# Performance work log

Hardware: AMD Instinct MI355X
Metric: run time of the kernel (lower is better)

Reference implementation:

```python
import jax, jax.numpy as jnp
import numpy as np

T, N, HID = 128, 128, 64
H_, W_ = 8, 8
CONV_OUT = H_ * W_ * HID  # 4096
N_SUB = 5
A, B, C = 5, 3, 6          # subtask_space = task_space.nvec[0]
SUB_SIZE = A + B + C       # 14
N_G = A * B * C            # 90
STATE = N_SUB + SUB_SIZE + HID + SUB_SIZE + 1 + 1  # 99
D_IN = CONV_OUT + 3 * N_SUB  # 4111


def setup_inputs() -> dict:
    key = jax.random.key(0)
    ks = jax.random.split(key, 16)
    sc = 0.02
    obs = jax.random.normal(ks[0], (T, N, CONV_OUT), jnp.float32)
    task_type = jax.random.randint(ks[1], (T, N, N_SUB), 0, A).astype(jnp.float32)
    count = jax.random.randint(ks[2], (T, N, N_SUB), 1, B + 1).astype(jnp.float32)
    obj = jax.random.randint(ks[3], (T, N, N_SUB), 0, C).astype(jnp.float32)
    inp = jnp.concatenate([obs, task_type, count, obj], axis=-1)  # [T,N,4111]
    hx = jnp.zeros((1, N, STATE), jnp.float32)
    return {
        "input": inp,
        "hx": hx,
        "Wf": jax.random.normal(ks[4], (HID, CONV_OUT + 2 * SUB_SIZE + 1), jnp.float32) * sc,
        "bf": jnp.zeros((HID,), jnp.float32),
        "Wih": jax.random.normal(ks[5], (3 * HID, 2 * HID), jnp.float32) * sc,
        "bih": jnp.zeros((3 * HID,), jnp.float32),
        "bhh": jnp.zeros((3 * HID,), jnp.float32),
        "Wc": jax.random.normal(ks[6], (1, 2 * HID), jnp.float32) * sc,
        "bc": jnp.zeros((1,), jnp.float32),
        "Wl": jax.random.normal(ks[7], (3, HID), jnp.float32) * sc,
        "bl": jnp.zeros((3,), jnp.float32),
        "Wpi": jax.random.normal(ks[8], (N_G, HID + SUB_SIZE), jnp.float32) * sc,
        "bpi": jnp.zeros((N_G,), jnp.float32),
        "Wb": jax.random.normal(ks[9], (2, CONV_OUT + SUB_SIZE), jnp.float32) * sc,
        "bb": jnp.zeros((2,), jnp.float32),
    }


def _forward(input, hx, Wf, bf, Wih, bih, bhh, Wc, bc, Wl, bl, Wpi, bpi, Wb, bb):
    obs = input[..., :CONV_OUT]
    tt = input[..., CONV_OUT:CONV_OUT + N_SUB].astype(jnp.int32)
    cnt = input[..., CONV_OUT + N_SUB:CONV_OUT + 2 * N_SUB].astype(jnp.int32) - 1
    obj = input[..., CONV_OUT + 2 * N_SUB:].astype(jnp.int32)

    ea, eb, ec = jnp.eye(A, dtype=input.dtype), jnp.eye(B, dtype=input.dtype), jnp.eye(C, dtype=input.dtype)

    def embed(t1, t2, t3):
        return jnp.concatenate([ea[t1], eb[t2], ec[t3]], axis=-1)

    M = embed(tt[0], cnt[0], obj[0])  # [N, N_SUB, SUB_SIZE]

    # parse hidden state
    h0_all = hx[0]
    i0, i1, i2, i3, i4 = np.cumsum([N_SUB, SUB_SIZE, HID, SUB_SIZE, 1])
    p0, r0, h0, g0, b0 = (h0_all[:, :i0], h0_all[:, i0:i1], h0_all[:, i1:i2],
                          h0_all[:, i2:i3], h0_all[:, i3:i4])

    new_ep = jnp.all(hx == 0)
    p0 = jnp.where(new_ep, p0.at[:, 0].set(1.0), p0)
    r0 = jnp.where(new_ep, M[:, 0], r0)
    g0 = jnp.where(new_ep, M[:, 0], g0)

    bhr, bhz, bhn = jnp.split(bhh, 3)
    keys = jax.random.split(jax.random.key(42), input.shape[0])

    def step(carry, xs):
        p_, r_, h_, g_, bprev = carry
        x, k = xs
        s = jnp.concatenate([x, r_, g_, bprev], axis=-1) @ Wf.T + bf   # f (linear)
        sh = jnp.concatenate([s, h_], axis=-1)
        cg = jax.nn.sigmoid(sh @ Wc.T + bc)                             # [N,1] phi_update
        # GRUCell called with hidden=None -> zero hidden state
        gi = sh @ Wih.T + bih
        gr, gz, gn = jnp.split(gi, 3, axis=-1)
        rg = jax.nn.sigmoid(gr + bhr)
        z = jax.nn.sigmoid(gz + bhz)
        n = jnp.tanh(gn + rg * bhn)
        hnew = (1.0 - z) * n
        # shift attention: per-batch conv1d(p, l, padding=1)
        l = jax.nn.softmax(h_ @ Wl.T + bl, axis=-1)                     # [N,3]
        pp = jnp.pad(p_, ((0, 0), (1, 1)))
        pconv = pp[:, :-2] * l[:, :1] + pp[:, 1:-1] * l[:, 1:2] + pp[:, 2:] * l[:, 2:]
        rnew = jnp.einsum('nk,nks->ns', pconv, M)
        p = cg * pconv + (1.0 - cg) * p_
        r = cg * rnew + (1.0 - cg) * r_
        h = cg * hnew + (1.0 - cg) * h_
        # pi_theta categorical over prod(subtask_space)
        lg = jnp.concatenate([h, r], axis=-1) @ Wpi.T + bpi
        k1, k2 = jax.random.split(k)
        g_idx = jax.random.categorical(k1, lg)                          # [N]
        lp_g = jnp.take_along_axis(jax.nn.log_softmax(lg, axis=-1), g_idx[:, None], axis=1)
        t1 = g_idx // (B * C)
        rem = g_idx % (B * C)
        gemb = embed(t1, rem // C, rem % C)                             # [N, SUB_SIZE]
        g = cg * gemb + (1.0 - cg) * g_
        # beta categorical over 2
        lbeta = jnp.concatenate([x, g], axis=-1) @ Wb.T + bb
        b_idx = jax.random.categorical(k2, lbeta)
        lp_b = jnp.take_along_axis(jax.nn.log_softmax(lbeta, axis=-1), b_idx[:, None], axis=1)
        bflt = b_idx[:, None].astype(p.dtype)
        out = jnp.concatenate([p, r, h, g, bflt, lp_g + lp_b], axis=-1)  # [N, STATE]
        return (p, r, h, g, bflt), out

    _, outs = jax.lax.scan(step, (p0, r0, h0, g0, b0), (obs, keys))
    return outs  # [T, N, STATE]


def reference(input, hx, Wf, bf, Wih, bih, bhh, Wc, bc, Wl, bl, Wpi, bpi, Wb, bb):
    outs = _forward(input, hx, Wf, bf, Wih, bih, bhh, Wc, bc, Wl, bl, Wpi, bpi, Wb, bb)
    return outs, outs[-1]
```

## Files before the change

### kernel.cpp

```cpp
#include <hip/hip_runtime.h>
#include <stdint.h>
#include <math.h>

#define T_STEPS 128
#define NB      128
#define HID     64
#define CONVOUT 4096
#define NSUB    5
#define SUBSZ   14
#define NG      90
#define STATE   99
#define DIN     4111
#define WFCOLS  4125
#define WBCOLS  4110
#define NROWS   (T_STEPS * NB)

__device__ __forceinline__ void tf2x32(unsigned k0, unsigned k1,
                                       unsigned x0, unsigned x1,
                                       unsigned &o0, unsigned &o1) {
  unsigned K0 = k0, K1 = k1, K2 = k0 ^ k1 ^ 0x1BD11BDAu;
  x0 += K0; x1 += K1;
  const int R0[4] = {13, 15, 26, 6};
  const int R1[4] = {17, 29, 16, 24};
  #pragma unroll
  for (int j = 0; j < 4; ++j) { x0 += x1; x1 = (x1 << R0[j]) | (x1 >> (32 - R0[j])); x1 ^= x0; }
  x0 += K1; x1 += K2 + 1u;
  #pragma unroll
  for (int j = 0; j < 4; ++j) { x0 += x1; x1 = (x1 << R1[j]) | (x1 >> (32 - R1[j])); x1 ^= x0; }
  x0 += K2; x1 += K0 + 2u;
  #pragma unroll
  for (int j = 0; j < 4; ++j) { x0 += x1; x1 = (x1 << R0[j]) | (x1 >> (32 - R0[j])); x1 ^= x0; }
  x0 += K0; x1 += K1 + 3u;
  #pragma unroll
  for (int j = 0; j < 4; ++j) { x0 += x1; x1 = (x1 << R1[j]) | (x1 >> (32 - R1[j])); x1 ^= x0; }
  x0 += K1; x1 += K2 + 4u;
  #pragma unroll
  for (int j = 0; j < 4; ++j) { x0 += x1; x1 = (x1 << R0[j]) | (x1 >> (32 - R0[j])); x1 ^= x0; }
  x0 += K2; x1 += K0 + 5u;
  o0 = x0; o1 = x1;
}

__device__ __forceinline__ double bits_to_gumbel_d(unsigned bits) {
  float f = __uint_as_float((bits >> 9) | 0x3f800000u) - 1.0f;
  const double tiny = (double)1.17549435e-38f;
  double u = fmax(tiny, (double)f + tiny);
  return -log(-log(u));
}

__device__ __forceinline__ float rlane(float v, int l) {
  return __int_as_float(__builtin_amdgcn_readlane(__float_as_int(v), l));
}

__device__ __forceinline__ void bar_lds() {
  __asm__ volatile("" ::: "memory");
  __builtin_amdgcn_s_waitcnt(0xC07F);
  __builtin_amdgcn_s_barrier();
  __asm__ volatile("" ::: "memory");
}

__global__ void k_transpose(const float* __restrict__ Wf, const float* __restrict__ Wb,
                            float* __restrict__ Wt) {
  int idx = blockIdx.x * 256 + threadIdx.x;
  int c = idx >> 12;
  int k = idx & 4095;
  float v = (c < 64) ? Wf[(size_t)c * WFCOLS + k] : Wb[(size_t)(c - 64) * WBCOLS + k];
  Wt[(size_t)k * 68 + c] = v;
}

__global__ __launch_bounds__(256, 4) void k_gemm(const float* __restrict__ inp,
                                                 const float* __restrict__ Wt,
                                                 float* __restrict__ Pf,
                                                 double* __restrict__ Pd) {
  __shared__ __align__(16) float xs[64 * 132];
  __shared__ double redd[2][64][2];
  int tid = threadIdx.x;
  int r = tid & 63;
  int w = __builtin_amdgcn_readfirstlane(tid >> 6);
  int rg = blockIdx.x >> 2, kq = blockIdx.x & 3;
  int rowbase = rg * 64;

  float acc[64];
  #pragma unroll
  for (int c = 0; c < 64; ++c) acc[c] = 0.f;
  double ad0 = 0.0, ad1 = 0.0;

  int s_rr[8], s_c4[8];
  #pragma unroll
  for (int i = 0; i < 8; ++i) {
    int idx = tid + i * 256;
    s_rr[i] = idx >> 5;
    s_c4[i] = idx & 31;
  }

  for (int kt = 0; kt < 8; ++kt) {
    int kb = kq * 1024 + kt * 128;
    #pragma unroll
    for (int i = 0; i < 8; ++i) {
      const float* g = inp + (size_t)(rowbase + s_rr[i]) * DIN + kb + s_c4[i] * 4;
      float4 v;
// ... 38 lines not shown
    float* d = red + (size_t)r * 65;
    #pragma unroll
    for (int c = 0; c < 64; ++c) d[c] = acc[c];
    redd[0][r][0] = ad0; redd[0][r][1] = ad1;
  }
  __syncthreads();
  if (w == 0) {
    const float* s = red + (size_t)r * 65;
    #pragma unroll
    for (int c = 0; c < 64; ++c) acc[c] += s[c];
    ad0 += redd[0][r][0]; ad1 += redd[0][r][1];
    int row = rowbase + r;
    float* po = Pf + (size_t)kq * NROWS * 64 + (size_t)row * 64;
    #pragma unroll
    for (int c = 0; c < 64; ++c) po[c] = acc[c];
    Pd[(size_t)kq * NROWS * 2 + (size_t)row * 2 + 0] = ad0;
    Pd[(size_t)kq * NROWS * 2 + (size_t)row * 2 + 1] = ad1;
  }
}

__global__ void k_reduce(const float* __restrict__ Pf, const double* __restrict__ Pd,
                         float* __restrict__ Xf, double* __restrict__ Xb) {
  size_t gid = (size_t)blockIdx.x * 256 + threadIdx.x;
  const size_t NF = (size_t)NROWS * 64;
  if (gid < NF) {
    Xf[gid] = (Pf[gid] + Pf[NF + gid]) + (Pf[2 * NF + gid] + Pf[3 * NF + gid]);
  } else if (gid < NF + (size_t)NROWS * 2) {
    size_t j = gid - NF;
    const size_t ND = (size_t)NROWS * 2;
    Xb[j] = (Pd[j] + Pd[ND + j]) + (Pd[2 * ND + j] + Pd[3 * ND + j]);
  }
}

__global__ void k_noise(double* __restrict__ Gg, double* __restrict__ Gb) {
  int t = blockIdx.x, tid = threadIdx.x;
  unsigned a, b, k1a, k1b, k2a, k2b, o0, o1;
  tf2x32(0u, 42u, 0u, (unsigned)t, a, b);
  tf2x32(a, b, 0u, 0u, k1a, k1b);
  tf2x32(a, b, 0u, 1u, k2a, k2b);
  for (int i = tid; i < NB * NG; i += 256) {
    tf2x32(k1a, k1b, 0u, (unsigned)i, o0, o1);
    Gg[(size_t)t * NB * NG + i] = bits_to_gumbel_d(o0 ^ o1);
  }
  {
    int i = tid;
    tf2x32(k2a, k2b, 0u, (unsigned)i, o0, o1);
    Gb[(size_t)t * NB * 2 + i] = bits_to_gumbel_d(o0 ^ o1);
  }
}

__global__ __launch_bounds__(256) void k_scan(
    const float* __restrict__ inp, const float* __restrict__ hx,
    const float* __restrict__ Wf, const float* __restrict__ bf,
    const float* __restrict__ Wih, const float* __restrict__ bih,
    const float* __restrict__ bhh, const float* __restrict__ Wc,
    const float* __restrict__ bc, const float* __restrict__ Wl,
    const float* __restrict__ bl, const float* __restrict__ Wpi,
    const float* __restrict__ bpi, const float* __restrict__ Wb,
    const float* __restrict__ bb,
    const float* __restrict__ Xf, const double* __restrict__ Xb,
    const double* __restrict__ Gg, const double* __restrict__ Gb,
    float* __restrict__ lgst, float* __restrict__ lbst,
    int* __restrict__ gidxst, int* __restrict__ bidxst,
    float* __restrict__ out) {
  const int n = blockIdx.x;
  const int tid = threadIdx.x;
  const int lane = tid & 63;
  const int w = __builtin_amdgcn_readfirstlane(tid >> 6);

  __shared__ float s_lds[64], h_lds[64], gi_lds[192];
  __shared__ int nz_sh;

  float wih_r[128];
  float bih_r = 0.f;
  if (w != 0) {
    int m = tid - 64;
    #pragma unroll
    for (int k = 0; k < 128; ++k) wih_r[k] = Wih[(size_t)m * 128 + k];
    bih_r = bih[m];
  }

  float wfs[29], wpi0[78], wpi1[78], mtr[5];
  float bf_r = 0, bhr_r = 0, bhz_r = 0, bhn_r = 0;
  float wc0 = 0, wc1 = 0, wl0 = 0, wl1 = 0, wl2 = 0;
  float bl0 = 0, bl1 = 0, bl2 = 0, bc0 = 0, bpi0 = 0, bpi1 = 0;
  float wbs0 = 0, wbs1 = 0;
  float hreg = 0.f, rgbp = 0.f, xf = 0.f;
  double S0 = 0.0, S1 = 0.0, bb0d = 0.0, bb1d = 0.0;
  double gum0 = 0.0, gum1 = 0.0, xb0 = 0.0, xb1 = 0.0, gb0 = 0.0, gb1 = 0.0;
  int dsto = -1;

  if (tid == 0) nz_sh = 0;
  __syncthreads();
  {
    int any = 0;
    const float4* h4 = (const float4*)hx;
    for (int i = tid; i < (NB * STATE) / 4; i += 256) {
      float4 v = h4[i];
      any |= (v.x != 0.f) | (v.y != 0.f) | (v.z != 0.f) | (v.w != 0.f);
    }
    if (any) nz_sh = 1;
  }
  if (w == 0) {
    #pragma unroll
    for (int k = 0; k < 29; ++k) wfs[k] = Wf[(size_t)lane * WFCOLS + CONVOUT + k];
    #pragma unroll
    for (int k = 0; k < 78; ++k) wpi0[k] = Wpi[(size_t)lane * 78 + k];
    bpi0 = bpi[lane];
    if (lane < 26) {
      #pragma unroll
      for (int k = 0; k < 78; ++k) wpi1[k] = Wpi[(size_t)(64 + lane) * 78 + k];
      bpi1 = bpi[64 + lane];
    }
    bf_r = bf[lane];
    bhr_r = bhh[lane]; bhz_r = bhh[64 + lane]; bhn_r = bhh[128 + lane];
    wc0 = Wc[lane]; wc1 = Wc[64 + lane]; bc0 = bc[0];
    wl0 = Wl[lane]; wl1 = Wl[64 + lane]; wl2 = Wl[128 + lane];
    bl0 = bl[0]; bl1 = bl[1]; bl2 = bl[2];
    bb0d = (double)bb[0]; bb1d = (double)bb[1];
    if (lane < 14) { wbs0 = Wb[CONVOUT + lane]; wbs1 = Wb[(size_t)WBCOLS + CONVOUT + lane]; }
    const float* r0 = inp + (size_t)n * DIN + CONVOUT;
    #pragma unroll
    for (int k = 0; k < 5; ++k) {
      int ttv = (int)r0[k], cntv = (int)r0[5 + k] - 1, objv = (int)r0[10 + k];
      float v = 0.f;
      if (lane < 5)       v = (lane == ttv) ? 1.f : 0.f;
      else if (lane < 8)  v = ((lane - 5) == cntv) ? 1.f : 0.f;
      else if (lane < 14) v = ((lane - 8) == objv) ? 1.f : 0.f;
      mtr[k] = v;
    }
    int src = -1;
    if (lane < 14)       { dsto = 5 + lane;          src = dsto; }
    else if (lane < 28)  { dsto = 83 + (lane - 14);  src = dsto; }
    else if (lane == 28) { dsto = 97;                src = 97; }
    else if (lane < 34)  { dsto = lane - 29;         src = dsto; }
    rgbp = (src >= 0) ? hx[(size_t)n * STATE + src] : 0.f;
    hreg = hx[(size_t)n * STATE + 19 + lane];
  }
  __syncthreads();
  if (w == 0) {
    if (nz_sh == 0) {
      const float* r0 = inp + (size_t)n * DIN + CONVOUT;
      int tt0 = (int)r0[0], cnt0 = (int)r0[5] - 1, obj0 = (int)r0[10];
      if (lane == 29) rgbp = 1.f;
      else if (lane < 14) rgbp = mtr[0];
      else if (lane >= 14 && lane < 28) {
        int j = lane - 14;
        rgbp = (j < 5) ? ((j == tt0) ? 1.f : 0.f)
             : (j < 8) ? (((j - 5) == cnt0) ? 1.f : 0.f)
                       : (((j - 8) == obj0) ? 1.f : 0.f);
      }
    }
    #pragma unroll
    for (int j = 0; j < 14; ++j) {
      double gv = (double)rlane(rgbp, 14 + j);
      S0 += gv * (double)rlane(wbs0, j);
      S1 += gv * (double)rlane(wbs1, j);
    }
    h_lds[lane] = hreg;
    gum0 = Gg[(size_t)n * NG + lane];
    gum1 = (lane < 26) ? Gg[(size_t)n * NG + 64 + lane] : 0.0;
    xf = Xf[(size_t)n * 64 + lane];
    xb0 = Xb[(size_t)n * 2 + 0]; xb1 = Xb[(size_t)n * 2 + 1];
    gb0 = Gb[(size_t)n * 2 + 0]; gb1 = Gb[(size_t)n * 2 + 1];
  }
  __syncthreads();

  const size_t outF = (size_t)T_STEPS * NB * STATE;

  #pragma unroll 1
  for (int t = 0; t < T_STEPS; ++t) {
    float sv_own = 0.f, cg = 0.f, accR0 = 0.f, accR1 = 0.f;
    double cgd = 0.0;

    if (w == 0) {
      float acc = xf + bf_r;
      #pragma unroll
      for (int k = 0; k < 29; ++k) acc = fmaf(wfs[k], rlane(rgbp, k), acc);
      sv_own = acc;
      s_lds[lane] = acc;
    }
    bar_lds();

    if (w == 0) {
      float p0 = wl0 * hreg, p1 = wl1 * hreg, p2 = wl2 * hreg;
      float cga = fmaf(wc1, hreg, wc0 * sv_own);
      #pragma unroll
      for (int off = 32; off; off >>= 1) {
        p0 += __shfl_xor(p0, off, 64);
        p1 += __shfl_xor(p1, off, 64);
        p2 += __shfl_xor(p2, off, 64);
        cga += __shfl_xor(cga, off, 64);
      }
      p0 += bl0; p1 += bl1; p2 += bl2;
      float mx = fmaxf(p0, fmaxf(p1, p2));
      float e0 = expf(p0 - mx), e1 = expf(p1 - mx), e2 = expf(p2 - mx);
      float se = e0 + e1 + e2;
      float l0 = e0 / se, l1 = e1 / se, l2 = e2 / se;
      cg = 1.f / (1.f + expf(-(cga + bc0)));
      cgd = (double)cg;
      float pv0 = rlane(rgbp, 29), pv1 = rlane(rgbp, 30), pv2 = rlane(rgbp, 31);
      float pv3 = rlane(rgbp, 32), pv4 = rlane(rgbp, 33);
      float pc0 = pv0 * l1 + pv1 * l2;
      float pc1 = pv0 * l0 + pv1 * l1 + pv2 * l2;
      float pc2 = pv1 * l0 + pv2 * l1 + pv3 * l2;
      float pc3 = pv2 * l0 + pv3 * l1 + pv4 * l2;
      float pc4 = pv3 * l0 + pv4 * l1;
      if (lane >= 29 && lane < 34) {
        float pcl = (lane == 29) ? pc0 : (lane == 30) ? pc1 : (lane == 31) ? pc2
                  : (lane == 32) ? pc3 : pc4;
        rgbp = cg * pcl + (1.f - cg) * rgbp;
      }
      if (lane < 14) {
        float rn = pc0 * mtr[0] + pc1 * mtr[1] + pc2 * mtr[2] + pc3 * mtr[3] + pc4 * mtr[4];
        rgbp = cg * rn + (1.f - cg) * rgbp;
      }
      #pragma unroll
      for (int k = 0; k < 14; ++k) {
        float rv = rlane(rgbp, k);
        accR0 = fmaf(wpi0[64 + k], rv, accR0);
        accR1 = fmaf(wpi1[64 + k], rv, accR1);
      }
    } else {
      float sv = s_lds[lane];
      float hv = h_lds[lane];
      float acc = bih_r;
      #pragma unroll
      for (int k = 0; k < 64; ++k) acc = fmaf(wih_r[k], rlane(sv, k), acc);
      #pragma unroll
      for (int k = 0; k < 64; ++k) acc = fmaf(wih_r[64 + k], rlane(hv, k), acc);
      gi_lds[tid - 64] = acc;
    }
    bar_lds();

    if (w == 0) {
      int tn = (t + 1 < T_STEPS) ? t + 1 : t;
      double gum0n = Gg[(size_t)tn * NB * NG + (size_t)n * NG + lane];
      double gum1n = (lane < 26) ? Gg[(size_t)tn * NB * NG + (size_t)n * NG + 64 + lane] : 0.0;
      float xfn = Xf[((size_t)tn * NB + n) * 64 + lane];
      double xb0n = Xb[((size_t)tn * NB + n) * 2 + 0];
      double xb1n = Xb[((size_t)tn * NB + n) * 2 + 1];
      double gb0n = Gb[((size_t)tn * NB + n) * 2 + 0];
      double gb1n = Gb[((size_t)tn * NB + n) * 2 + 1];

      float g0 = gi_lds[lane], g1 = gi_lds[64 + lane], g2 = gi_lds[128 + lane];
      float rg = 1.f / (1.f + expf(-(g0 + bhr_r)));
      float z  = 1.f / (1.f + expf(-(g1 + bhz_r)));
      float nn = tanhf(g2 + rg * bhn_r);
      float hnew = (1.f - z) * nn;
      hreg = cg * hnew + (1.f - cg) * hreg;

      float a0 = bpi0 + accR0, a1 = bpi1 + accR1;
      #pragma unroll
      for (int k = 0; k < 64; ++k) {
        float hv2 = rlane(hreg, k);
        a0 = fmaf(wpi0[k], hv2, a0);
        a1 = fmaf(wpi1[k], hv2, a1);
      }
      const float NEGINF = -3.0e38f;
      float vb0 = (float)(gum0 + (double)a0);
      float vb1 = (lane < 26) ? (float)(gum1 + (double)a1) : NEGINF;
      float m1, m2; int idx;
      if (vb1 > vb0) { m1 = vb1; idx = lane + 64; m2 = vb0; }
      else           { m1 = vb0; idx = lane;      m2 = vb1; }
      #pragma unroll
      for (int off = 32; off; off >>= 1) {
        float o1 = __shfl_xor(m1, off, 64);
        int   oi = __shfl_xor(idx, off, 64);
        float o2 = __shfl_xor(m2, off, 64);
        bool take = (o1 > m1) || (o1 == m1 && oi < idx);
        float base2 = take ? m1 : m2;
        float oth   = take ? o2 : o1;
        m2 = fmaxf(base2, oth);
        if (take) { m1 = o1; idx = oi; }
      }
      int gidx = idx;
      if (m1 - m2 < 3e-5f) {
        double e0d = (double)bpi0;
        double e1d = (lane < 26) ? (double)bpi1 : -1.0e300;
        #pragma unroll 1
        for (int k = 0; k < 64; ++k) {
          double hv2 = (double)rlane(hreg, k);
          e0d = fma((double)Wpi[(size_t)lane * 78 + k], hv2, e0d);
          if (lane < 26) e1d = fma((double)Wpi[(size_t)(64 + lane) * 78 + k], hv2, e1d);
        }
        #pragma unroll 1
        for (int k = 0; k < 14; ++k) {
          double rv = (double)rlane(rgbp, k);
          e0d = fma((double)Wpi[(size_t)lane * 78 + 64 + k], rv, e0d);
          if (lane < 26) e1d = fma((double)Wpi[(size_t)(64 + lane) * 78 + 64 + k], rv, e1d);
        }
        double kk0 = e0d + gum0;
        double kk1 = (lane < 26) ? e1d + gum1 : -1.0e300;
        double d1; int di;
        if (kk1 > kk0) { d1 = kk1; di = lane + 64; } else { d1 = kk0; di = lane; }
        #pragma unroll
        for (int off = 32; off; off >>= 1) {
          double od = __shfl_xor(d1, off, 64);
          int    oi = __shfl_xor(di, off, 64);
          if (od > d1 || (od == d1 && oi < di)) { d1 = od; di = oi; }
        }
        gidx = di;
      }
      int t1 = gidx / 18, rem = gidx - t1 * 18;
      int b1 = rem / 6, c1 = rem - b1 * 6;
      if (lane >= 14 && lane < 28) {
        int j = lane - 14;
        float ge = (j < 5) ? ((j == t1) ? 1.f : 0.f)
                 : (j < 8) ? (((j - 5) == b1) ? 1.f : 0.f)
                           : (((j - 8) == c1) ? 1.f : 0.f);
        rgbp = cg * ge + (1.f - cg) * rgbp;
      }
      double u0 = (double)rlane(wbs0, t1) + (double)rlane(wbs0, 5 + b1) + (double)rlane(wbs0, 8 + c1);
      double u1 = (double)rlane(wbs1, t1) + (double)rlane(wbs1, 5 + b1) + (double)rlane(wbs1, 8 + c1);
      S0 = cgd * u0 + (1.0 - cgd) * S0;
      S1 = cgd * u1 + (1.0 - cgd) * S1;
      double lb0 = xb0 + bb0d + S0;
      double lb1 = xb1 + bb1d + S1;
      int bi = ((lb1 + gb1) > (lb0 + gb0)) ? 1 : 0;
      if (lane == 28) rgbp = (float)bi;

      size_t rn = (size_t)t * NB + n;
      float* ob = out + rn * STATE;
      if (dsto >= 0) ob[dsto] = rgbp;
      ob[19 + lane] = hreg;
      lgst[rn * NG + lane] = a0;
      if (lane < 26) lgst[rn * NG + 64 + lane] = a1;
      if (lane == 0) {
        lbst[rn * 2 + 0] = (float)lb0; lbst[rn * 2 + 1] = (float)lb1;
        gidxst[rn] = gidx; bidxst[rn] = bi;
      }
      if (t == T_STEPS - 1) {
        float* of = out + outF + (size_t)n * STATE;
        if (dsto >= 0) of[dsto] = rgbp;
        of[19 + lane] = hreg;
      }
      h_lds[lane] = hreg;
      gum0 = gum0n; gum1 = gum1n; xf = xfn;
      xb0 = xb0n; xb1 = xb1n; gb0 = gb0n; gb1 = gb1n;
    }
  }
}

__global__ __launch_bounds__(256) void k_lp(const float* __restrict__ lgst,
                                            const float* __restrict__ lbst,
                                            const int* __restrict__ gidxst,
                                            const int* __restrict__ bidxst,
                                            float* __restrict__ out) {
  int tid = threadIdx.x, lane = tid & 63, w = tid >> 6;
  size_t rn = (size_t)blockIdx.x * 4 + w;
  const float* lg = lgst + rn * NG;
  float v0 = lg[lane];
  float v1 = (lane < 26) ? lg[64 + lane] : -3.0e38f;
  float ml = fmaxf(v0, v1);
  #pragma unroll
  for (int off = 32; off; off >>= 1) ml = fmaxf(ml, __shfl_xor(ml, off, 64));
  float e = expf(v0 - ml) + ((lane < 26) ? expf(v1 - ml) : 0.f);
  #pragma unroll
  for (int off = 32; off; off >>= 1) e += __shfl_xor(e, off, 64);
  int gi = gidxst[rn];
  float lpg = (lg[gi] - ml) - logf(e);
  float lb0 = lbst[rn * 2 + 0], lb1 = lbst[rn * 2 + 1];
  int bi = bidxst[rn];
  float mx = fmaxf(lb0, lb1);
  float seb = expf(lb0 - mx) + expf(lb1 - mx);
  float lpb = ((bi ? lb1 : lb0) - mx) - logf(seb);
  if (lane == 0) {
    int t = (int)(rn / NB), n = (int)(rn % NB);
    float lp = lpg + lpb;
    out[rn * STATE + 98] = lp;
    if (t == T_STEPS - 1) out[(size_t)T_STEPS * NB * STATE + (size_t)n * STATE + 98] = lp;
  }
}

extern "C" void kernel_launch(void* const* d_in, const int* in_sizes, int n_in,
                              void* d_out, int out_size, void* d_ws, size_t ws_size,
                              hipStream_t stream) {
  const float* inp = (const float*)d_in[0];
  const float* hx  = (const float*)d_in[1];
  const float* Wf  = (const float*)d_in[2];
  const float* bf  = (const float*)d_in[3];
  const float* Wih = (const float*)d_in[4];
  const float* bih = (const float*)d_in[5];
  const float* bhh = (const float*)d_in[6];
  const float* Wc  = (const float*)d_in[7];
  const float* bc  = (const float*)d_in[8];
  const float* Wl  = (const float*)d_in[9];
  const float* bl  = (const float*)d_in[10];
  const float* Wpi = (const float*)d_in[11];
  const float* bpi = (const float*)d_in[12];
  const float* Wb  = (const float*)d_in[13];
  const float* bb  = (const float*)d_in[14];
  float* out = (float*)d_out;

  double* Gg = (double*)d_ws;
  double* Gb = Gg + (size_t)T_STEPS * NB * NG;
  double* Xb = Gb + (size_t)T_STEPS * NB * 2;
  double* Pd = Xb + (size_t)NROWS * 2;
  float*  Wt = (float*)(Pd + (size_t)4 * NROWS * 2);
  float*  Xf = Wt + (size_t)4096 * 68;
  float*  Pf = Xf + (size_t)NROWS * 64;
  float*  lgst = Pf;
  float*  lbst = lgst + (size_t)NROWS * NG;
  int*    gidxst = (int*)(lbst + (size_t)NROWS * 2);
  int*    bidxst = gidxst + NROWS;

  k_transpose<<<(66 * 4096) / 256, 256, 0, stream>>>(Wf, Wb, Wt);
  k_gemm<<<1024, 256, 0, stream>>>(inp, Wt, Pf, Pd);
  {
    size_t tot = (size_t)NROWS * 64 + (size_t)NROWS * 2;
    k_reduce<<<(int)((tot + 255) / 256), 256, 0, stream>>>(Pf, Pd, Xf, Xb);
  }
  k_noise<<<T_STEPS, 256, 0, stream>>>(Gg, Gb);
  k_scan<<<NB, 256, 0, stream>>>(inp, hx, Wf, bf, Wih, bih, bhh, Wc, bc, Wl, bl,
                                 Wpi, bpi, Wb, bb, Xf, Xb, Gg, Gb,
                                 lgst, lbst, gidxst, bidxst, out);
  k_lp<<<NROWS / 4, 256, 0, stream>>>(lgst, lbst, gidxst, bidxst, out);
}
```

Measured before the change: 963.0 us.

## Precompute input-side GRU gates by GEMM and restructure scan waves with DPP reductions

Adds a second GEMM that computes the time-invariant part of the GRU input gates (Wih·(x+bf)) and the critic term for all timesteps ahead of the serial scan. The recurrent contributions of r and g are folded in algebraically through small precomputed projections, so they no longer cost a full matvec per step. The policy logits and argmax are spread across three waves and reduced with DPP, and the noise kernel launches more blocks. The aim is to shorten the serial per-step critical path, at the cost of extra kernels, workspace aliasing and float-rounding differences that could affect ties in the sampled indices.

Result: no change. 944.8 us (-1.9%).

```diff
diff --git a/kernel.cpp b/kernel.cpp
--- a/kernel.cpp
+++ b/kernel.cpp
@@ -14,6 +14,15 @@
 #define WFCOLS  4125
 #define WBCOLS  4110
 #define NROWS   (T_STEPS * NB)
+#define GIXST   193
+
+#define NEGINFF (-3.0e38f)
+
+typedef __attribute__((ext_vector_type(2))) float f32x2;
+
+#define SEL5(a,b,c,d,e,ix) ((ix)==0?(a):(ix)==1?(b):(ix)==2?(c):(ix)==3?(d):(e))
+#define SEL3(a,b,c,ix)     ((ix)==0?(a):(ix)==1?(b):(c))
+#define SEL6(a,b,c,d,e,f,ix) ((ix)==0?(a):(ix)==1?(b):(ix)==2?(c):(ix)==3?(d):(ix)==4?(e):(f))
 
 __device__ __forceinline__ void tf2x32(unsigned k0, unsigned k1,
                                        unsigned x0, unsigned x1,
@@ -51,6 +60,36 @@
   return __int_as_float(__builtin_amdgcn_readlane(__float_as_int(v), l));
 }
 
+template<int CTRL, int RM>
+__device__ __forceinline__ float dpp_mv(float x, float fill) {
+  return __int_as_float(__builtin_amdgcn_update_dpp(
+      __float_as_int(fill), __float_as_int(x), CTRL, RM, 0xF, false));
+}
+
+__device__ __forceinline__ void dpp_sum4(float &a, float &b, float &c, float &d) {
+  #define S4(C, RM) { a += dpp_mv<C,RM>(a,0.f); b += dpp_mv<C,RM>(b,0.f); \
+                      c += dpp_mv<C,RM>(c,0.f); d += dpp_mv<C,RM>(d,0.f); }
+  S4(0x111,0xF) S4(0x112,0xF) S4(0x114,0xF) S4(0x118,0xF) S4(0x142,0xA) S4(0x143,0xC)
+  #undef S4
+}
+
+__device__ __forceinline__ void dpp_amax2(float &m1, float &m2) {
+  #define A2(C, RM) { float o1 = dpp_mv<C,RM>(m1,NEGINFF), o2 = dpp_mv<C,RM>(m2,NEGINFF); \
+    m2 = fmaxf(fmaxf(m2,o2), fminf(m1,o1)); m1 = fmaxf(m1,o1); }
+  A2(0x111,0xF) A2(0x112,0xF) A2(0x114,0xF) A2(0x118,0xF) A2(0x142,0xA) A2(0x143,0xC)
+  #undef A2
+}
+
+__device__ __forceinline__ float dpp_sum_bcast(float v) {
+  v += dpp_mv<0x111,0xF>(v, 0.f);
+  v += dpp_mv<0x112,0xF>(v, 0.f);
+  v += dpp_mv<0x114,0xF>(v, 0.f);
+  v += dpp_mv<0x118,0xF>(v, 0.f);
+  v += dpp_mv<0x142,0xA>(v, 0.f);
+  v += dpp_mv<0x143,0xC>(v, 0.f);
+  return rlane(v, 63);
+}
+
 __device__ __forceinline__ void bar_lds() {
   __asm__ volatile("" ::: "memory");
   __builtin_amdgcn_s_waitcnt(0xC07F);
@@ -65,6 +104,14 @@
   int k = idx & 4095;
   float v = (c < 64) ? Wf[(size_t)c * WFCOLS + k] : Wb[(size_t)(c - 64) * WBCOLS + k];
   Wt[(size_t)k * 68 + c] = v;
+}
+
+__global__ void k_tr2(const float* __restrict__ Wih, const float* __restrict__ Wc,
+                      float* __restrict__ Wt2) {
+  int idx = blockIdx.x * 256 + threadIdx.x;
+  if (idx >= 64 * GIXST) return;
+  int k = idx / GIXST, i = idx - k * GIXST;
+  Wt2[(size_t)k * 208 + i] = (i < 192) ? Wih[(size_t)i * 128 + k] : Wc[k];
 }
 
 __global__ __launch_bounds__(256, 4) void k_gemm(const float* __restrict__ inp,
@@ -169,33 +216,74 @@
   }
 }
 
+__global__ __launch_bounds__(256) void k_gemm2(const float* __restrict__ Xf,
+                                               const float* __restrict__ bf,
+                                               const float* __restrict__ Wt2,
+                                               float* __restrict__ GIx) {
+  int tid = threadIdx.x;
+  int lane = tid & 63;
+  int w = __builtin_amdgcn_readfirstlane(tid >> 6);
+  int row = blockIdx.x * 64 + lane;
+  int i0 = w * 48;
+
+  float x[64];
+  const float* xr = Xf + (size_t)row * 64;
+  #pragma unroll
+  for (int k4 = 0; k4 < 16; ++k4) {
+    float4 xv = *(const float4*)&xr[k4 * 4];
+    float4 bv = *(const float4*)&bf[k4 * 4];
+    x[k4 * 4 + 0] = xv.x + bv.x;
+    x[k4 * 4 + 1] = xv.y + bv.y;
+    x[k4 * 4 + 2] = xv.z + bv.z;
+    x[k4 * 4 + 3] = xv.w + bv.w;
+  }
+  float acc[48];
+  #pragma unroll
+  for (int j = 0; j < 48; ++j) acc[j] = 0.f;
+  float acc48 = 0.f;
+  for (int k = 0; k < 64; ++k) {
+    const float* wp = Wt2 + (size_t)k * 208 + i0;
+    float xk = x[k];
+    #pragma unroll
+    for (int j = 0; j < 48; ++j) acc[j] = fmaf(xk, wp[j], acc[j]);
+    if (w == 3) acc48 = fmaf(xk, wp[48], acc48);
+  }
+  float* o = GIx + (size_t)row * GIXST + i0;
+  #pragma unroll
+  for (int j = 0; j < 48; ++j) o[j] = acc[j];
+  if (w == 3) o[48] = acc48;
+}
+
 __global__ void k_noise(double* __restrict__ Gg, double* __restrict__ Gb) {
-  int t = blockIdx.x, tid = threadIdx.x;
-  unsigned a, b, k1a, k1b, k2a, k2b, o0, o1;
-  tf2x32(0u, 42u, 0u, (unsigned)t, a, b);
-  tf2x32(a, b, 0u, 0u, k1a, k1b);
-  tf2x32(a, b, 0u, 1u, k2a, k2b);
-  for (int i = tid; i < NB * NG; i += 256) {
-    tf2x32(k1a, k1b, 0u, (unsigned)i, o0, o1);
-    Gg[(size_t)t * NB * NG + i] = bits_to_gumbel_d(o0 ^ o1);
-  }
-  {
-    int i = tid;
-    tf2x32(k2a, k2b, 0u, (unsigned)i, o0, o1);
-    Gb[(size_t)t * NB * 2 + i] = bits_to_gumbel_d(o0 ^ o1);
+  int b = blockIdx.x;
+  int t = b / 9, c = b - t * 9;
+  int tid = threadIdx.x;
+  unsigned a, bk, k1a, k1b, k2a, k2b, o0, o1;
+  tf2x32(0u, 42u, 0u, (unsigned)t, a, bk);
+  if (c < 8) {
+    tf2x32(a, bk, 0u, 0u, k1a, k1b);
+    int i0 = c * 1440;
+    for (int i = i0 + tid; i < i0 + 1440; i += 256) {
+      tf2x32(k1a, k1b, 0u, (unsigned)i, o0, o1);
+      Gg[(size_t)t * NB * NG + i] = bits_to_gumbel_d(o0 ^ o1);
+    }
+  } else {
+    tf2x32(a, bk, 0u, 1u, k2a, k2b);
+    tf2x32(k2a, k2b, 0u, (unsigned)tid, o0, o1);
+    Gb[(size_t)t * NB * 2 + tid] = bits_to_gumbel_d(o0 ^ o1);
   }
 }
 
 __global__ __launch_bounds__(256) void k_scan(
     const float* __restrict__ inp, const float* __restrict__ hx,
-    const float* __restrict__ Wf, const float* __restrict__ bf,
+    const float* __restrict__ Wf,
     const float* __restrict__ Wih, const float* __restrict__ bih,
     const float* __restrict__ bhh, const float* __restrict__ Wc,
     const float* __restrict__ bc, const float* __restrict__ Wl,
     const float* __restrict__ bl, const float* __restrict__ Wpi,
     const float* __restrict__ bpi, const float* __restrict__ Wb,
     const float* __restrict__ bb,
-    const float* __restrict__ Xf, const double* __restrict__ Xb,
+    const float* __restrict__ GIx, const double* __restrict__ Xb,
     const double* __restrict__ Gg, const double* __restrict__ Gb,
     float* __restrict__ lgst, float* __restrict__ lbst,
     int* __restrict__ gidxst, int* __restrict__ bidxst,
@@ -205,35 +293,62 @@
   const int lane = tid & 63;
   const int w = __builtin_amdgcn_readfirstlane(tid >> 6);
 
-  __shared__ float s_lds[64], h_lds[64], gi_lds[192];
-  __shared__ int nz_sh;
-
-  float wih_r[128];
-  float bih_r = 0.f;
-  if (w != 0) {
-    int m = tid - 64;
-    #pragma unroll
-    for (int k = 0; k < 128; ++k) wih_r[k] = Wih[(size_t)m * 128 + k];
-    bih_r = bih[m];
-  }
-
-  float wfs[29], wpi0[78], wpi1[78], mtr[5];
-  float bf_r = 0, bhr_r = 0, bhz_r = 0, bhn_r = 0;
+  __shared__ __align__(16) float h_lds[64];
+  __shared__ __align__(16) float gi_lds[192];
+  __shared__ float pq_lds[4];
+  __shared__ float cp_lds[2][8];
+  __shared__ float pm_lds[3][2];
+  __shared__ int   pidx_lds[3];
+  __shared__ int   pub_i[4];
+  __shared__ float pub_f[2];
+  __shared__ int   nz_sh;
+  __shared__ float ws_lds[29][64];
+  __shared__ float rg0_lds[32];
+  __shared__ int   ti_lds[16];
+
+  const int i = tid - 64;
+  const int oi = (w >= 1) ? (w - 1) * 30 + lane : 0;
+
+  f32x2 wih_h[32];
+  f32x2 wpi_p[32];
+  float bihc = 0.f, bpi_r = 0.f;
+  float Mg[14], V[5], WpiM[5];
+  float m_b = 0.f, GI_r = 0.f, GI_g = 0.f, accR = 0.f, gihreg = 0.f;
+  float gixA = 0.f;
+  double gumA = 0.0, gumB = 0.0;
+  #pragma unroll
+  for (int j = 0; j < 14; ++j) Mg[j] = 0.f;
+  #pragma unroll
+  for (int k = 0; k < 5; ++k) { V[k] = 0.f; WpiM[k] = 0.f; }
+
+  float rgbp = 0.f, hreg = 0.f;
+  float mtr[5];
+  float bhr_r = 0, bhz_r = 0, bhn_r = 0;
   float wc0 = 0, wc1 = 0, wl0 = 0, wl1 = 0, wl2 = 0;
-  float bl0 = 0, bl1 = 0, bl2 = 0, bc0 = 0, bpi0 = 0, bpi1 = 0;
+  float bl0 = 0, bl1 = 0, bl2 = 0, bc0 = 0;
   float wbs0 = 0, wbs1 = 0;
-  float hreg = 0.f, rgbp = 0.f, xf = 0.f;
+  float kap[5], wg[14], wcB = 0.f;
+  float cR = 0.f, cG = 0.f, CXa = 0.f;
   double S0 = 0.0, S1 = 0.0, bb0d = 0.0, bb1d = 0.0;
-  double gum0 = 0.0, gum1 = 0.0, xb0 = 0.0, xb1 = 0.0, gb0 = 0.0, gb1 = 0.0;
+  double xb0 = 0.0, xb1 = 0.0, gb0 = 0.0, gb1 = 0.0;
+  double xb0n = 0.0, xb1n = 0.0, gb0n = 0.0, gb1n = 0.0;
   int dsto = -1;
+  int ttk[5], cnk[5], obk[5];
+  float wfs[29];
+  #pragma unroll
+  for (int k = 0; k < 5; ++k) { mtr[k] = 0.f; kap[k] = 0.f; ttk[k] = 0; cnk[k] = 0; obk[k] = 0; }
+  #pragma unroll
+  for (int j = 0; j < 14; ++j) wg[j] = 0.f;
+  #pragma unroll
+  for (int k = 0; k < 29; ++k) wfs[k] = 0.f;
 
   if (tid == 0) nz_sh = 0;
   __syncthreads();
   {
     int any = 0;
     const float4* h4 = (const float4*)hx;
-    for (int i = tid; i < (NB * STATE) / 4; i += 256) {
-      float4 v = h4[i];
+    for (int q = tid; q < (NB * STATE) / 4; q += 256) {
+      float4 v = h4[q];
       any |= (v.x != 0.f) | (v.y != 0.f) | (v.z != 0.f) | (v.w != 0.f);
     }
     if (any) nz_sh = 1;
@@ -241,15 +356,6 @@
   if (w == 0) {
     #pragma unroll
     for (int k = 0; k < 29; ++k) wfs[k] = Wf[(size_t)lane * WFCOLS + CONVOUT + k];
-    #pragma unroll
-    for (int k = 0; k < 78; ++k) wpi0[k] = Wpi[(size_t)lane * 78 + k];
-    bpi0 = bpi[lane];
-    if (lane < 26) {
-      #pragma unroll
-      for (int k = 0; k < 78; ++k) wpi1[k] = Wpi[(size_t)(64 + lane) * 78 + k];
-      bpi1 = bpi[64 + lane];
-    }
-    bf_r = bf[lane];
     bhr_r = bhh[lane]; bhz_r = bhh[64 + lane]; bhn_r = bhh[128 + lane];
     wc0 = Wc[lane]; wc1 = Wc[64 + lane]; bc0 = bc[0];
     wl0 = Wl[lane]; wl1 = Wl[64 + lane]; wl2 = Wl[128 + lane];
@@ -260,11 +366,13 @@
     #pragma unroll
     for (int k = 0; k < 5; ++k) {
       int ttv = (int)r0[k], cntv = (int)r0[5 + k] - 1, objv = (int)r0[10 + k];
+      ttk[k] = ttv; cnk[k] = cntv; obk[k] = objv;
       float v = 0.f;
       if (lane < 5)       v = (lane == ttv) ? 1.f : 0.f;
       else if (lane < 8)  v = ((lane - 5) == cntv) ? 1.f : 0.f;
       else if (lane < 14) v = ((lane - 8) == objv) ? 1.f : 0.f;
       mtr[k] = v;
+      if (lane == 0) { ti_lds[k] = ttv; ti_lds[5 + k] = cntv; ti_lds[10 + k] = objv; }
     }
     int src = -1;
     if (lane < 14)       { dsto = 5 + lane;          src = dsto; }
@@ -275,18 +383,48 @@
     hreg = hx[(size_t)n * STATE + 19 + lane];
   }
   __syncthreads();
+
   if (w == 0) {
     if (nz_sh == 0) {
-      const float* r0 = inp + (size_t)n * DIN + CONVOUT;
-      int tt0 = (int)r0[0], cnt0 = (int)r0[5] - 1, obj0 = (int)r0[10];
       if (lane == 29) rgbp = 1.f;
       else if (lane < 14) rgbp = mtr[0];
       else if (lane >= 14 && lane < 28) {
         int j = lane - 14;
-        rgbp = (j < 5) ? ((j == tt0) ? 1.f : 0.f)
-             : (j < 8) ? (((j - 5) == cnt0) ? 1.f : 0.f)
-                       : (((j - 8) == obj0) ? 1.f : 0.f);
-      }
+        rgbp = (j < 5) ? ((j == ttk[0]) ? 1.f : 0.f)
+             : (j < 8) ? (((j - 5) == cnk[0]) ? 1.f : 0.f)
+                       : (((j - 8) == obk[0]) ? 1.f : 0.f);
+      }
+    }
+    #pragma unroll
+    for (int j = 0; j < 29; ++j) ws_lds[j][lane] = wfs[j];
+    if (lane < 28) rg0_lds[lane] = rgbp;
+    if (lane == 28) { rg0_lds[28] = rgbp; pub_f[0] = rgbp; }
+    h_lds[lane] = hreg;
+    if (lane < 6) cp_lds[1][lane] = 0.f;
+    if (lane < 3) pub_i[lane] = 0;
+  }
+  __syncthreads();
+
+  if (w == 0) {
+    #pragma unroll
+    for (int k = 0; k < 5; ++k) {
+      float wfrm = SEL5(wfs[0], wfs[1], wfs[2], wfs[3], wfs[4], ttk[k])
+                 + SEL3(wfs[5], wfs[6], wfs[7], cnk[k])
+                 + SEL6(wfs[8], wfs[9], wfs[10], wfs[11], wfs[12], wfs[13], obk[k]);
+      kap[k] = dpp_sum_bcast(wc0 * wfrm);
+    }
+    #pragma unroll
+    for (int j = 0; j < 14; ++j) wg[j] = dpp_sum_bcast(wc0 * wfs[14 + j]);
+    wcB = dpp_sum_bcast(wc0 * wfs[28]);
+    {
+      float rs = 0.f, gs = 0.f;
+      #pragma unroll
+      for (int j = 0; j < 14; ++j) {
+        rs = fmaf(wfs[j], rlane(rgbp, j), rs);
+        gs = fmaf(wfs[14 + j], rlane(rgbp, 14 + j), gs);
+      }
+      cR = dpp_sum_bcast(wc0 * rs);
+      cG = dpp_sum_bcast(wc0 * gs);
     }
     #pragma unroll
     for (int j = 0; j < 14; ++j) {
@@ -294,46 +432,98 @@
       S0 += gv * (double)rlane(wbs0, j);
       S1 += gv * (double)rlane(wbs1, j);
     }
-    h_lds[lane] = hreg;
-    gum0 = Gg[(size_t)n * NG + lane];
-    gum1 = (lane < 26) ? Gg[(size_t)n * NG + 64 + lane] : 0.0;
-    xf = Xf[(size_t)n * 64 + lane];
+    CXa = GIx[((size_t)0 * NB + n) * GIXST + 192];
     xb0 = Xb[(size_t)n * 2 + 0]; xb1 = Xb[(size_t)n * 2 + 1];
     gb0 = Gb[(size_t)n * 2 + 0]; gb1 = Gb[(size_t)n * 2 + 1];
+    float p0 = wl0 * hreg, p1 = wl1 * hreg, p2 = wl2 * hreg, cah = wc1 * hreg;
+    dpp_sum4(p0, p1, p2, cah);
+    if (lane == 63) { pq_lds[0] = p0; pq_lds[1] = p1; pq_lds[2] = p2; pq_lds[3] = cah; }
+  } else {
+    float wsrow[64];
+    {
+      const f32x2* wr0 = (const f32x2*)&Wih[(size_t)i * 128];
+      #pragma unroll
+      for (int l2 = 0; l2 < 32; ++l2) { f32x2 v = wr0[l2]; wsrow[2*l2] = v.x; wsrow[2*l2+1] = v.y; }
+    }
+    float Mr[14];
+    #pragma unroll
+    for (int j = 0; j < 14; ++j) Mr[j] = 0.f;
+    #pragma unroll
+    for (int l = 0; l < 64; ++l) {
+      float wv = wsrow[l];
+      #pragma unroll
+      for (int j = 0; j < 14; ++j) {
+        Mr[j] = fmaf(wv, ws_lds[j][l], Mr[j]);
+        Mg[j] = fmaf(wv, ws_lds[14 + j][l], Mg[j]);
+      }
+      m_b = fmaf(wv, ws_lds[28][l], m_b);
+    }
+    #pragma unroll
+    for (int k = 0; k < 5; ++k) {
+      int tt = ti_lds[k], cn = ti_lds[5 + k], ob = ti_lds[10 + k];
+      V[k] = SEL5(Mr[0], Mr[1], Mr[2], Mr[3], Mr[4], tt)
+           + SEL3(Mr[5], Mr[6], Mr[7], cn)
+           + SEL6(Mr[8], Mr[9], Mr[10], Mr[11], Mr[12], Mr[13], ob);
+    }
+    GI_r = 0.f; GI_g = 0.f;
+    #pragma unroll
+    for (int j = 0; j < 14; ++j) {
+      GI_r = fmaf(Mr[j], rg0_lds[j], GI_r);
+      GI_g = fmaf(Mg[j], rg0_lds[14 + j], GI_g);
+    }
+    {
+      const f32x2* wr = (const f32x2*)&Wih[(size_t)i * 128 + 64];
+      #pragma unroll
+      for (int k2 = 0; k2 < 32; ++k2) wih_h[k2] = wr[k2];
+      bihc = bih[i];
+    }
+    if (lane < 30) {
+      const f32x2* pr = (const f32x2*)&Wpi[(size_t)oi * 78];
+      #pragma unroll
+      for (int k2 = 0; k2 < 32; ++k2) wpi_p[k2] = pr[k2];
+      bpi_r = bpi[oi];
+      const float* wp = Wpi + (size_t)oi * 78 + 64;
+      #pragma unroll
+      for (int k = 0; k < 5; ++k)
+        WpiM[k] = wp[ti_lds[k]] + wp[5 + ti_lds[5 + k]] + wp[8 + ti_lds[10 + k]];
+      accR = 0.f;
+      #pragma unroll
+      for (int j = 0; j < 14; ++j) accR = fmaf(wp[j], rg0_lds[j], accR);
+      gumA = Gg[(size_t)n * NG + oi];
+    }
+    gixA = GIx[((size_t)0 * NB + n) * GIXST + i];
+    {
+      const f32x2* hp = (const f32x2*)h_lds;
+      f32x2 A = {bihc, 0.f}, B = {0.f, 0.f};
+      #pragma unroll
+      for (int k2 = 0; k2 < 32; k2 += 2) {
+        f32x2 h0 = hp[k2], h1 = hp[k2 + 1];
+        A.x = fmaf(wih_h[k2].x, h0.x, A.x);
+        A.y = fmaf(wih_h[k2].y, h0.y, A.y);
+        B.x = fmaf(wih_h[k2 + 1].x, h1.x, B.x);
+        B.y = fmaf(wih_h[k2 + 1].y, h1.y, B.y);
+      }
+      gihreg = (A.x + A.y) + (B.x + B.y);
+    }
   }
   __syncthreads();
 
   const size_t outF = (size_t)T_STEPS * NB * STATE;
+
+  float cg = 0.f;
+  double cgd = 0.0;
 
   #pragma unroll 1
   for (int t = 0; t < T_STEPS; ++t) {
-    float sv_own = 0.f, cg = 0.f, accR0 = 0.f, accR1 = 0.f;
-    double cgd = 0.0;
-
     if (w == 0) {
-      float acc = xf + bf_r;
-      #pragma unroll
-      for (int k = 0; k < 29; ++k) acc = fmaf(wfs[k], rlane(rgbp, k), acc);
-      sv_own = acc;
-      s_lds[lane] = acc;
-    }
-    bar_lds();
-
-    if (w == 0) {
-      float p0 = wl0 * hreg, p1 = wl1 * hreg, p2 = wl2 * hreg;
-      float cga = fmaf(wc1, hreg, wc0 * sv_own);
-      #pragma unroll
-      for (int off = 32; off; off >>= 1) {
-        p0 += __shfl_xor(p0, off, 64);
-        p1 += __shfl_xor(p1, off, 64);
-        p2 += __shfl_xor(p2, off, 64);
-        cga += __shfl_xor(cga, off, 64);
-      }
-      p0 += bl0; p1 += bl1; p2 += bl2;
-      float mx = fmaxf(p0, fmaxf(p1, p2));
-      float e0 = expf(p0 - mx), e1 = expf(p1 - mx), e2 = expf(p2 - mx);
+      float P0 = pq_lds[0] + bl0, P1v = pq_lds[1] + bl1, P2v = pq_lds[2] + bl2;
+      float cgaH = pq_lds[3];
+      float mx = fmaxf(P0, fmaxf(P1v, P2v));
+      float e0 = expf(P0 - mx), e1 = expf(P1v - mx), e2 = expf(P2v - mx);
       float se = e0 + e1 + e2;
       float l0 = e0 / se, l1 = e1 / se, l2 = e2 / se;
+      float bprev = rlane(rgbp, 28);
+      float cga = CXa + cR + cG + bprev * wcB + cgaH;
       cg = 1.f / (1.f + expf(-(cga + bc0)));
       cgd = (double)cg;
       float pv0 = rlane(rgbp, 29), pv1 = rlane(rgbp, 30), pv2 = rlane(rgbp, 31);
@@ -349,72 +539,104 @@
         rgbp = cg * pcl + (1.f - cg) * rgbp;
       }
       if (lane < 14) {
-        float rn = pc0 * mtr[0] + pc1 * mtr[1] + pc2 * mtr[2] + pc3 * mtr[3] + pc4 * mtr[4];
-        rgbp = cg * rn + (1.f - cg) * rgbp;
-      }
-      #pragma unroll
-      for (int k = 0; k < 14; ++k) {
-        float rv = rlane(rgbp, k);
-        accR0 = fmaf(wpi0[64 + k], rv, accR0);
-        accR1 = fmaf(wpi1[64 + k], rv, accR1);
+        float rn2 = pc0 * mtr[0] + pc1 * mtr[1] + pc2 * mtr[2] + pc3 * mtr[3] + pc4 * mtr[4];
+        rgbp = cg * rn2 + (1.f - cg) * rgbp;
+      }
+      cR = cg * (pc0 * kap[0] + pc1 * kap[1] + pc2 * kap[2] + pc3 * kap[3] + pc4 * kap[4])
+         + (1.f - cg) * cR;
+      if (lane == 0) {
+        float* cp = cp_lds[t & 1];
+        cp[0] = cg; cp[1] = pc0; cp[2] = pc1; cp[3] = pc2; cp[4] = pc3; cp[5] = pc4;
       }
     } else {
-      float sv = s_lds[lane];
-      float hv = h_lds[lane];
-      float acc = bih_r;
-      #pragma unroll
-      for (int k = 0; k < 64; ++k) acc = fmaf(wih_r[k], rlane(sv, k), acc);
-      #pragma unroll
-      for (int k = 0; k < 64; ++k) acc = fmaf(wih_r[64 + k], rlane(hv, k), acc);
-      gi_lds[tid - 64] = acc;
+      const float* cp = cp_lds[(t + 1) & 1];
+      float cgp = cp[0];
+      float rmix = cp[1] * V[0] + cp[2] * V[1] + cp[3] * V[2] + cp[4] * V[3] + cp[5] * V[4];
+      GI_r = cgp * rmix + (1.f - cgp) * GI_r;
+      int pt1 = pub_i[0], pb1 = pub_i[1], pc1i = pub_i[2];
+      float mgs = SEL5(Mg[0], Mg[1], Mg[2], Mg[3], Mg[4], pt1)
+                + SEL3(Mg[5], Mg[6], Mg[7], pb1)
+                + SEL6(Mg[8], Mg[9], Mg[10], Mg[11], Mg[12], Mg[13], pc1i);
+      GI_g = cgp * mgs + (1.f - cgp) * GI_g;
+      float bprev = pub_f[0];
+      gi_lds[i] = gihreg + gixA + GI_r + GI_g + bprev * m_b;
     }
     bar_lds();
 
     if (w == 0) {
-      int tn = (t + 1 < T_STEPS) ? t + 1 : t;
-      double gum0n = Gg[(size_t)tn * NB * NG + (size_t)n * NG + lane];
-      double gum1n = (lane < 26) ? Gg[(size_t)tn * NB * NG + (size_t)n * NG + 64 + lane] : 0.0;
-      float xfn = Xf[((size_t)tn * NB + n) * 64 + lane];
-      double xb0n = Xb[((size_t)tn * NB + n) * 2 + 0];
-      double xb1n = Xb[((size_t)tn * NB + n) * 2 + 1];
-      double gb0n = Gb[((size_t)tn * NB + n) * 2 + 0];
-      double gb1n = Gb[((size_t)tn * NB + n) * 2 + 1];
-
       float g0 = gi_lds[lane], g1 = gi_lds[64 + lane], g2 = gi_lds[128 + lane];
       float rg = 1.f / (1.f + expf(-(g0 + bhr_r)));
       float z  = 1.f / (1.f + expf(-(g1 + bhz_r)));
       float nn = tanhf(g2 + rg * bhn_r);
-      float hnew = (1.f - z) * nn;
-      hreg = cg * hnew + (1.f - cg) * hreg;
-
-      float a0 = bpi0 + accR0, a1 = bpi1 + accR1;
-      #pragma unroll
-      for (int k = 0; k < 64; ++k) {
-        float hv2 = rlane(hreg, k);
-        a0 = fmaf(wpi0[k], hv2, a0);
-        a1 = fmaf(wpi1[k], hv2, a1);
-      }
-      const float NEGINF = -3.0e38f;
-      float vb0 = (float)(gum0 + (double)a0);
-      float vb1 = (lane < 26) ? (float)(gum1 + (double)a1) : NEGINF;
-      float m1, m2; int idx;
-      if (vb1 > vb0) { m1 = vb1; idx = lane + 64; m2 = vb0; }
-      else           { m1 = vb0; idx = lane;      m2 = vb1; }
-      #pragma unroll
-      for (int off = 32; off; off >>= 1) {
-        float o1 = __shfl_xor(m1, off, 64);
-        int   oi = __shfl_xor(idx, off, 64);
-        float o2 = __shfl_xor(m2, off, 64);
-        bool take = (o1 > m1) || (o1 == m1 && oi < idx);
-        float base2 = take ? m1 : m2;
-        float oth   = take ? o2 : o1;
-        m2 = fmaxf(base2, oth);
-        if (take) { m1 = o1; idx = oi; }
-      }
-      int gidx = idx;
-      if (m1 - m2 < 3e-5f) {
-        double e0d = (double)bpi0;
-        double e1d = (lane < 26) ? (double)bpi1 : -1.0e300;
+      hreg = cg * ((1.f - z) * nn) + (1.f - cg) * hreg;
+      h_lds[lane] = hreg;
+    } else {
+      int tn = (t + 1 < T_STEPS) ? t + 1 : t;
+      gixA = GIx[((size_t)tn * NB + n) * GIXST + i];
+      if (lane < 30) gumB = Gg[(size_t)tn * NB * NG + (size_t)n * NG + oi];
+    }
+    bar_lds();
+
+    if (w != 0) {
+      const float* cp = cp_lds[t & 1];
+      float cgc = cp[0];
+      float vb = NEGINFF;
+      if (lane < 30) {
+        float rmx = cp[1] * WpiM[0] + cp[2] * WpiM[1] + cp[3] * WpiM[2]
+                  + cp[4] * WpiM[3] + cp[5] * WpiM[4];
+        accR = cgc * rmx + (1.f - cgc) * accR;
+        const f32x2* hp = (const f32x2*)h_lds;
+        f32x2 A = {bpi_r + accR, 0.f}, B = {0.f, 0.f};
+        #pragma unroll
+        for (int k2 = 0; k2 < 32; k2 += 2) {
+          f32x2 h0 = hp[k2], h1 = hp[k2 + 1];
+          A.x = fmaf(wpi_p[k2].x, h0.x, A.x);
+          A.y = fmaf(wpi_p[k2].y, h0.y, A.y);
+          B.x = fmaf(wpi_p[k2 + 1].x, h1.x, B.x);
+          B.y = fmaf(wpi_p[k2 + 1].y, h1.y, B.y);
+        }
+        float lgv = (A.x + A.y) + (B.x + B.y);
+        lgst[((size_t)t * NB + n) * NG + oi] = lgv;
+        vb = (float)(gumA + (double)lgv);
+      }
+      gumA = gumB;
+      float m1 = vb, m2 = NEGINFF;
+      dpp_amax2(m1, m2);
+      float M1w = rlane(m1, 63);
+      unsigned long long bm = __ballot(vb == M1w);
+      int il = __ffsll(bm) - 1;
+      if (lane == 63) { pm_lds[w - 1][0] = m1; pm_lds[w - 1][1] = m2; pidx_lds[w - 1] = il; }
+    } else {
+      float p0 = wl0 * hreg, p1 = wl1 * hreg, p2 = wl2 * hreg, cah = wc1 * hreg;
+      dpp_sum4(p0, p1, p2, cah);
+      if (lane == 63) { pq_lds[0] = p0; pq_lds[1] = p1; pq_lds[2] = p2; pq_lds[3] = cah; }
+      size_t rn = (size_t)t * NB + n;
+      float* ob = out + rn * STATE;
+      ob[19 + lane] = hreg;
+      if (dsto >= 0 && (lane < 14 || lane >= 29)) ob[dsto] = rgbp;
+      int tn = (t + 1 < T_STEPS) ? t + 1 : t;
+      CXa = GIx[((size_t)tn * NB + n) * GIXST + 192];
+      xb0n = Xb[((size_t)tn * NB + n) * 2 + 0];
+      xb1n = Xb[((size_t)tn * NB + n) * 2 + 1];
+      gb0n = Gb[((size_t)tn * NB + n) * 2 + 0];
+      gb1n = Gb[((size_t)tn * NB + n) * 2 + 1];
+    }
+    bar_lds();
+
+    if (w == 0) {
+      float m1a = pm_lds[0][0], m2a = pm_lds[0][1];
+      float m1b = pm_lds[1][0], m2b = pm_lds[1][1];
+      float m1c = pm_lds[2][0], m2c = pm_lds[2][1];
+      float M1 = fmaxf(m1a, fmaxf(m1b, m1c));
+      float M2; int gidx;
+      if (m1a == M1)      { M2 = fmaxf(m2a, fmaxf(m1b, m1c)); gidx = pidx_lds[0]; }
+      else if (m1b == M1) { M2 = fmaxf(m2b, fmaxf(m1a, m1c)); gidx = 30 + pidx_lds[1]; }
+      else                { M2 = fmaxf(m2c, fmaxf(m1a, m1b)); gidx = 60 + pidx_lds[2]; }
+      if (M1 - M2 < 3e-5f) {
+        double gum0s = Gg[(size_t)t * NB * NG + (size_t)n * NG + lane];
+        double gum1s = (lane < 26) ? Gg[(size_t)t * NB * NG + (size_t)n * NG + 64 + lane] : 0.0;
+        double e0d = (double)bpi[lane];
+        double e1d = (lane < 26) ? (double)bpi[64 + lane] : -1.0e300;
         #pragma unroll 1
         for (int k = 0; k < 64; ++k) {
           double hv2 = (double)rlane(hreg, k);
@@ -427,15 +649,15 @@
           e0d = fma((double)Wpi[(size_t)lane * 78 + 64 + k], rv, e0d);
           if (lane < 26) e1d = fma((double)Wpi[(size_t)(64 + lane) * 78 + 64 + k], rv, e1d);
         }
-        double kk0 = e0d + gum0;
-        double kk1 = (lane < 26) ? e1d + gum1 : -1.0e300;
+        double kk0 = e0d + gum0s;
+        double kk1 = (lane < 26) ? e1d + gum1s : -1.0e300;
         double d1; int di;
         if (kk1 > kk0) { d1 = kk1; di = lane + 64; } else { d1 = kk0; di = lane; }
         #pragma unroll
         for (int off = 32; off; off >>= 1) {
           double od = __shfl_xor(d1, off, 64);
-          int    oi = __shfl_xor(di, off, 64);
-          if (od > d1 || (od == d1 && oi < di)) { d1 = od; di = oi; }
+          int    oid = __shfl_xor(di, off, 64);
+          if (od > d1 || (od == d1 && oid < di)) { d1 = od; di = oid; }
         }
         gidx = di;
       }
@@ -448,6 +670,10 @@
                            : (((j - 8) == c1) ? 1.f : 0.f);
         rgbp = cg * ge + (1.f - cg) * rgbp;
       }
+      float wgs = SEL5(wg[0], wg[1], wg[2], wg[3], wg[4], t1)
+                + SEL3(wg[5], wg[6], wg[7], b1)
+                + SEL6(wg[8], wg[9], wg[10], wg[11], wg[12], wg[13], c1);
+      cG = cg * wgs + (1.f - cg) * cG;
       double u0 = (double)rlane(wbs0, t1) + (double)rlane(wbs0, 5 + b1) + (double)rlane(wbs0, 8 + c1);
       double u1 = (double)rlane(wbs1, t1) + (double)rlane(wbs1, 5 + b1) + (double)rlane(wbs1, 8 + c1);
       S0 = cgd * u0 + (1.0 - cgd) * S0;
@@ -456,26 +682,35 @@
       double lb1 = xb1 + bb1d + S1;
       int bi = ((lb1 + gb1) > (lb0 + gb0)) ? 1 : 0;
       if (lane == 28) rgbp = (float)bi;
-
       size_t rn = (size_t)t * NB + n;
       float* ob = out + rn * STATE;
-      if (dsto >= 0) ob[dsto] = rgbp;
-      ob[19 + lane] = hreg;
-      lgst[rn * NG + lane] = a0;
-      if (lane < 26) lgst[rn * NG + 64 + lane] = a1;
+      if (dsto >= 0 && lane >= 14 && lane < 29) ob[dsto] = rgbp;
       if (lane == 0) {
         lbst[rn * 2 + 0] = (float)lb0; lbst[rn * 2 + 1] = (float)lb1;
         gidxst[rn] = gidx; bidxst[rn] = bi;
-      }
+        pub_i[0] = t1; pub_i[1] = b1; pub_i[2] = c1;
+      }
+      if (lane == 28) pub_f[0] = rgbp;
       if (t == T_STEPS - 1) {
         float* of = out + outF + (size_t)n * STATE;
         if (dsto >= 0) of[dsto] = rgbp;
         of[19 + lane] = hreg;
       }
-      h_lds[lane] = hreg;
-      gum0 = gum0n; gum1 = gum1n; xf = xfn;
       xb0 = xb0n; xb1 = xb1n; gb0 = gb0n; gb1 = gb1n;
-    }
+    } else {
+      const f32x2* hp = (const f32x2*)h_lds;
+      f32x2 A = {bihc, 0.f}, B = {0.f, 0.f};
+      #pragma unroll
+      for (int k2 = 0; k2 < 32; k2 += 2) {
+        f32x2 h0 = hp[k2], h1 = hp[k2 + 1];
+        A.x = fmaf(wih_h[k2].x, h0.x, A.x);
+        A.y = fmaf(wih_h[k2].y, h0.y, A.y);
+        B.x = fmaf(wih_h[k2 + 1].x, h1.x, B.x);
+        B.y = fmaf(wih_h[k2 + 1].y, h1.y, B.y);
+      }
+      gihreg = (A.x + A.y) + (B.x + B.y);
+    }
+    bar_lds();
   }
 }
 
@@ -530,27 +765,31 @@
   const float* bb  = (const float*)d_in[14];
   float* out = (float*)d_out;
 
-  double* Gg = (double*)d_ws;
-  double* Gb = Gg + (size_t)T_STEPS * NB * NG;
-  double* Xb = Gb + (size_t)T_STEPS * NB * 2;
-  double* Pd = Xb + (size_t)NROWS * 2;
-  float*  Wt = (float*)(Pd + (size_t)4 * NROWS * 2);
-  float*  Xf = Wt + (size_t)4096 * 68;
-  float*  Pf = Xf + (size_t)NROWS * 64;
-  float*  lgst = Pf;
+  double* Gg  = (double*)d_ws;
+  double* Gb  = Gg + (size_t)T_STEPS * NB * NG;
+  double* Xb  = Gb + (size_t)T_STEPS * NB * 2;
+  double* Pd  = Xb + (size_t)NROWS * 2;
+  float*  Wt  = (float*)(Pd + (size_t)4 * NROWS * 2);
+  float*  Wt2 = Wt + (size_t)4096 * 68;
+  float*  Xf  = Wt2 + (size_t)64 * 208;
+  float*  Pf  = Xf + (size_t)NROWS * 64;
+  float*  GIx = Pf;
+  float*  lgst = (float*)Pd;
   float*  lbst = lgst + (size_t)NROWS * NG;
   int*    gidxst = (int*)(lbst + (size_t)NROWS * 2);
   int*    bidxst = gidxst + NROWS;
 
   k_transpose<<<(66 * 4096) / 256, 256, 0, stream>>>(Wf, Wb, Wt);
+  k_tr2<<<(64 * GIXST + 255) / 256, 256, 0, stream>>>(Wih, Wc, Wt2);
   k_gemm<<<1024, 256, 0, stream>>>(inp, Wt, Pf, Pd);
   {
     size_t tot = (size_t)NROWS * 64 + (size_t)NROWS * 2;
     k_reduce<<<(int)((tot + 255) / 256), 256, 0, stream>>>(Pf, Pd, Xf, Xb);
   }
-  k_noise<<<T_STEPS, 256, 0, stream>>>(Gg, Gb);
-  k_scan<<<NB, 256, 0, stream>>>(inp, hx, Wf, bf, Wih, bih, bhh, Wc, bc, Wl, bl,
-                                 Wpi, bpi, Wb, bb, Xf, Xb, Gg, Gb,
+  k_gemm2<<<256, 256, 0, stream>>>(Xf, bf, Wt2, GIx);
+  k_noise<<<T_STEPS * 9, 256, 0, stream>>>(Gg, Gb);
+  k_scan<<<NB, 256, 0, stream>>>(inp, hx, Wf, Wih, bih, bhh, Wc, bc, Wl, bl,
+                                 Wpi, bpi, Wb, bb, GIx, Xb, Gg, Gb,
                                  lgst, lbst, gidxst, bidxst, out);
   k_lp<<<NROWS / 4, 256, 0, stream>>>(lgst, lbst, gidxst, bidxst, out);
 }
```
